# Kernel tuning notes

Measured on AMD Instinct MI355X. Metric: run time of the kernel, lower is better.

The kernel has to match this reference:

```python
import jax, jax.numpy as jnp
import numpy as np

B, N, C, H = 2, 2048, 128, 4
C4 = C // 4


def setup_inputs() -> dict:
    key = jax.random.key(0)
    ks = jax.random.split(key, 20)
    s = 0.02
    f = lambda k, sh: (jax.random.normal(k, sh, jnp.float32) * s)
    return {
        'x': jax.random.normal(ks[0], (B, N, C), jnp.float32),
        'A': jax.random.randint(ks[1], (N, N), 0, 2).astype(jnp.int32),
        'q_w1': f(ks[2], (C, C)), 'kv_w1': f(ks[3], (2 * C, C)),
        'proj_w1': f(ks[4], (C, C)), 'proj_b1': jnp.zeros((C,), jnp.float32),
        'q_w2': f(ks[5], (C, C)), 'kv_w2': f(ks[6], (2 * C, C)),
        'proj_w2': f(ks[7], (C, C)), 'proj_b2': jnp.zeros((C,), jnp.float32),
        'cq_w': f(ks[8], (C4, C)), 'cq_b': jnp.zeros((C4,), jnp.float32),
        'ck_w': f(ks[9], (C4, C)), 'ck_b': jnp.zeros((C4,), jnp.float32),
        'cv_w': f(ks[10], (C, C)), 'cv_b': jnp.zeros((C,), jnp.float32),
        'gc_w': f(ks[11], (C, C)), 'gc_b': jnp.zeros((C,), jnp.float32),
    }


def _attn_block(x, A, qw, kvw, pw, pb):
    # Attention._inner_attention + residual; qkv_bias=False, scale=head_dim**-0.5
    b, n, c = x.shape
    hd = c // H
    q = (x @ qw.T).reshape(b, n, H, hd).transpose(0, 2, 1, 3)          # [B,H,N,hd]
    kv = (x @ kvw.T).reshape(b, n, 2, H, hd).transpose(2, 0, 3, 1, 4)  # [2,B,H,N,hd]
    k, v = kv[0], kv[1]
    attn = jnp.einsum('bhnd,bhmd->bhnm', q, k) * (hd ** -0.5)
    attn = jnp.where(A[None, None] > 0, attn, jnp.float32(-9e15))
    attn = jax.nn.softmax(attn, axis=-1)
    out = jnp.einsum('bhnm,bhmd->bhnd', attn, v).transpose(0, 2, 1, 3).reshape(b, n, c)
    return out @ pw.T + pb + x


def _graph_conv(x, cq_w, cq_b, ck_w, ck_b, cv_w, cv_b, gc_w, gc_b):
    # GraphConvolution.forward: conv1d(k=1) QKV, softmax, topk scatter mask, masked softmax, bmm
    b, s, c = x.shape
    xp = x.transpose(0, 2, 1)                                          # [B,C,N]
    query = jnp.einsum('oi,bin->bon', cq_w, xp) + cq_b[:, None]        # [B,C/4,N]
    keyt = (jnp.einsum('oi,bin->bon', ck_w, xp) + ck_b[:, None]).transpose(0, 2, 1)  # [B,N,C/4]
    adj = jax.nn.softmax(jnp.einsum('bnc,bcm->bnm', keyt, query), axis=-1)           # [B,N,N]
    kk = int(s / 3 * 2)                                                # top-2/3 per row
    _, idx = jax.lax.top_k(adj, kk)                                    # [B,N,kk]
    mask = jnp.zeros(adj.shape, bool).at[
        jnp.arange(b)[:, None, None], jnp.arange(s)[None, :, None], idx].set(True)
    adj = jax.nn.softmax(jnp.where(mask, adj, -jnp.inf), axis=-1)
    value = (jnp.einsum('oi,bin->bon', cv_w, xp) + cv_b[:, None]).transpose(0, 2, 1)  # [B,N,C]
    support = value @ gc_w
    return jnp.einsum('bnm,bmc->bnc', adj, support) + gc_b


def reference(x, A, q_w1, kv_w1, proj_w1, proj_b1, q_w2, kv_w2, proj_w2, proj_b2,
              cq_w, cq_b, ck_w, ck_b, cv_w, cv_b, gc_w, gc_b):
    x = _attn_block(x, A, q_w1, kv_w1, proj_w1, proj_b1)
    x = _attn_block(x, A, q_w2, kv_w2, proj_w2, proj_b2)
    return _graph_conv(x, cq_w, cq_b, ck_w, ck_b, cv_w, cv_b, gc_w, gc_b)
```

## Files before the change

kernel.cpp:

```cpp
#include <hip/hip_runtime.h>
#include <hip/hip_bf16.h>
#include <math.h>

#define KK_TOP 1365

typedef __attribute__((ext_vector_type(8))) short v8s;
typedef __attribute__((ext_vector_type(4))) float f32x4;

#define MFMA16(a, b, c) __builtin_amdgcn_mfma_f32_16x16x32_bf16(a, b, c, 0, 0, 0)

__device__ inline float wave_max_f(float v) {
    #pragma unroll
    for (int m = 1; m < 64; m <<= 1) v = fmaxf(v, __shfl_xor(v, m));
    return v;
}
__device__ inline float wave_min_f(float v) {
    #pragma unroll
    for (int m = 1; m < 64; m <<= 1) v = fminf(v, __shfl_xor(v, m));
    return v;
}
__device__ inline float wave_sum_f(float v) {
    #pragma unroll
    for (int m = 1; m < 64; m <<= 1) v += __shfl_xor(v, m);
    return v;
}
__device__ inline unsigned short bf16bits(float x) {
    __hip_bfloat16 h = __float2bfloat16(x);
    return *reinterpret_cast<unsigned short*>(&h);
}

__global__ __launch_bounds__(256) void prep_k(
    const int* __restrict__ A, unsigned* __restrict__ Ab2,
    const float* __restrict__ cv_w, const float* __restrict__ cv_b,
    const float* __restrict__ gc_w, float* __restrict__ MT, float* __restrict__ B2,
    const float* __restrict__ x, short* __restrict__ xb,
    const float* __restrict__ q_w1, const float* __restrict__ kv_w1,
    const float* __restrict__ proj_w1, const float* __restrict__ q_w2,
    const float* __restrict__ kv_w2, const float* __restrict__ proj_w2,
    short* __restrict__ WALLb)
{
    const int bx = blockIdx.x;
    if (bx < 512) {
        const int lane = threadIdx.x & 63;
        const int w = threadIdx.x >> 6;
        const int row = bx * 4 + w;
        const int* rp = A + (size_t)row * 2048;
        for (int i = 0; i < 32; ++i) {
            unsigned long long bal = __ballot(rp[i * 64 + lane] > 0);
            if (lane == 0)  Ab2[(size_t)row * 64 + 2 * i]     = (unsigned)bal;
            if (lane == 32) Ab2[(size_t)row * 64 + 2 * i + 1] = (unsigned)(bal >> 32);
        }
    } else if (bx < 576) {
        const int b2 = bx - 512;
        const int c = b2 * 2 + (threadIdx.x >> 7);
        const int k = threadIdx.x & 127;
        float a = 0.f;
        #pragma unroll 4
        for (int i = 0; i < 128; ++i)
            a += cv_w[(size_t)i * 128 + k] * gc_w[(size_t)i * 128 + c];
        MT[(size_t)c * 128 + k] = a;
        if (b2 == 0 && threadIdx.x < 128) {
            float s = 0.f;
            #pragma unroll 4
            for (int i = 0; i < 128; ++i)
                s += cv_b[i] * gc_w[(size_t)i * 128 + threadIdx.x];
            B2[threadIdx.x] = s;
        }
    } else if (bx < 640) {
        const size_t base = (size_t)(bx - 576) * 8192;
        #pragma unroll 8
        for (int i = 0; i < 32; ++i) {
            size_t e = base + threadIdx.x + i * 256;
            xb[e] = (short)bf16bits(x[e]);
        }
    } else {
        const int base = (bx - 640) * 8192;
        const float* src; int off;
        if (base < 16384)       { src = q_w1;    off = base; }
        else if (base < 49152)  { src = kv_w1;   off = base - 16384; }
        else if (base < 65536)  { src = proj_w1; off = base - 49152; }
        else if (base < 81920)  { src = q_w2;    off = base - 65536; }
        else if (base < 114688) { src = kv_w2;   off = base - 81920; }
        else                    { src = proj_w2; off = base - 114688; }
        short* dst = WALLb + base;
        #pragma unroll 8
        for (int i = 0; i < 32; ++i) {
            int e = threadIdx.x + i * 256;
            dst[e] = (short)bf16bits(src[off + e]);
        }
    }
}

enum { MODE_QKV = 0, MODE_PROJ = 1 };

template <int MODE, bool EMITB>
__global__ __launch_bounds__(256) void mfma_gemm_k(
    const short* __restrict__ Xb, const short* __restrict__ Wb,
    const float* __restrict__ bias, const float* __restrict__ resid,
    short* __restrict__ Qo, short* __restrict__ Ko, short* __restrict__ Vto,
    float* __restrict__ Fo, short* __restrict__ Bo)
{
    const int tid = threadIdx.x;
    const int w = tid >> 6, lane = tid & 63;
    const int g = lane >> 4, c = lane & 15;
    const int m0 = blockIdx.x * 64 + w * 16;
    const int nbase = blockIdx.y * 64;

    v8s af[4];
    #pragma unroll
    for (int kk = 0; kk < 4; ++kk)
        af[kk] = *(const v8s*)(Xb + (size_t)(m0 + c) * 128 + kk * 32 + g * 8);

    for (int nf = 0; nf < 4; ++nf) {
        const int n0 = nbase + nf * 16;
        f32x4 acc = {0.f, 0.f, 0.f, 0.f};
        #pragma unroll
        for (int kk = 0; kk < 4; ++kk) {
            v8s bfr = *(const v8s*)(Wb + (size_t)(n0 + c) * 128 + kk * 32 + g * 8);
            acc = MFMA16(af[kk], bfr, acc);
        }
        const int ccol = n0 + c;
        #pragma unroll
        for (int r = 0; r < 4; ++r) {
            const int m = m0 + 4 * g + r;
            const int b = m >> 11, n = m & 2047;
            if (MODE == MODE_QKV) {
                unsigned short hv = bf16bits(acc[r]);
                if (ccol < 128) {
                    int hh = ccol >> 5, d = ccol & 31;
                    Qo[((size_t)(b * 4 + hh) * 2048 + n) * 32 + d] = (short)hv;
                } else if (ccol < 256) {
                    int c2 = ccol - 128; int hh = c2 >> 5, d = c2 & 31;
                    Ko[((size_t)(b * 4 + hh) * 2048 + n) * 32 + d] = (short)hv;
                } else {
                    int c2 = ccol - 256; int hh = c2 >> 5, d = c2 & 31;
                    Vto[((size_t)(b * 4 + hh) * 32 + d) * 2048 + n] = (short)hv;
                }
            } else {
                float v = acc[r] + bias[ccol] + resid[(size_t)m * 128 + ccol];
                Fo[(size_t)m * 128 + ccol] = v;
                if (EMITB) Bo[(size_t)m * 128 + ccol] = (short)bf16bits(v);
            }
        }
    }
}

__global__ __launch_bounds__(256) void graphmm_k(
    const float* __restrict__ X, const float* __restrict__ cq_w,
    const float* __restrict__ cq_b, const float* __restrict__ ck_w,
    const float* __restrict__ ck_b, const float* __restrict__ MT,
    const float* __restrict__ B2, float* __restrict__ QgT,
    float* __restrict__ Kg, __hip_bfloat16* __restrict__ SUPt)
{
    __shared__ __align__(16) float Xs[64][132];
    __shared__ __align__(16) float Ws[32][132];
    const int tid = threadIdx.x;
    const int m0 = blockIdx.x * 64;
    const int y = blockIdx.y;
    const float* W0   = (y == 0) ? cq_w : (y == 1) ? ck_w : MT;
    const float* bias = (y == 0) ? cq_b : (y == 1) ? ck_b : B2;
    const int n0 = (y < 2) ? 0 : (y - 2) * 32;

    #pragma unroll
    for (int i = 0; i < 32; ++i) {
        int idx = tid + i * 256;
        int row = idx >> 7, col = idx & 127;
        Xs[row][col] = X[(size_t)(m0 + row) * 128 + col];
    }
    #pragma unroll
    for (int i = 0; i < 16; ++i) {
        int idx = tid + i * 256;
        int r = idx >> 7, col = idx & 127;
        Ws[r][col] = W0[(size_t)(n0 + r) * 128 + col];
    }
    __syncthreads();

    const int r = tid >> 4;
    const int c = tid & 15;
    float acc[4][2] = {{0.f, 0.f}, {0.f, 0.f}, {0.f, 0.f}, {0.f, 0.f}};

    #pragma unroll
    for (int k = 0; k < 128; k += 4) {
        float4 w0 = *(const float4*)&Ws[c][k];
        float4 w1 = *(const float4*)&Ws[c + 16][k];
        #pragma unroll
        for (int i = 0; i < 4; ++i) {
            float4 xv = *(const float4*)&Xs[r + 16 * i][k];
            acc[i][0] += xv.x * w0.x + xv.y * w0.y + xv.z * w0.z + xv.w * w0.w;
            acc[i][1] += xv.x * w1.x + xv.y * w1.y + xv.z * w1.z + xv.w * w1.w;
        }
    }

    #pragma unroll
    for (int i = 0; i < 4; ++i) {
        int m = m0 + r + 16 * i;
        int b = m >> 11, n = m & 2047;
        #pragma unroll
        for (int jj = 0; jj < 2; ++jj) {
            int ccol = n0 + c + 16 * jj;
            float v = acc[i][jj];
            if (y == 0) {
                QgT[((size_t)b * 32 + ccol) * 2048 + n] = v + bias[ccol];
            } else if (y == 1) {
                Kg[(size_t)m * 32 + ccol] = v + bias[ccol];
            } else {
                SUPt[((size_t)b * 128 + ccol) * 2048 + n] = __float2bfloat16(v + bias[ccol]);
            }
        }
    }
}

__global__ __launch_bounds__(512, 8) void attn_mfma_k(
    const short* __restrict__ Qb, const short* __restrict__ Kb,
    const short* __restrict__ Vt, const unsigned* __restrict__ Ab2,
    short* __restrict__ Ob)
{
    __shared__ __align__(16) float OLDS[8][64][8];
    __shared__ float lred[8][16];

    const int tid = threadIdx.x;
    const int w = tid >> 6, lane = tid & 63;
    const int g = lane >> 4, c = lane & 15;
    const int bb = 4 * g;
    const int wg = blockIdx.x;
    const int b = wg >> 9, h = (wg >> 7) & 3, r0w = (wg & 127) << 4;
    const int bh = b * 4 + h;

    const v8s qf = *(const v8s*)(Qb + ((size_t)bh * 2048 + r0w + c) * 32 + g * 8);
    const short* Kp = Kb + (size_t)bh * 2048 * 32;
    const short* Vp = Vt + (size_t)bh * 32 * 2048;
    const unsigned* Mrow = Ab2 + (size_t)(r0w + c) * 64;

    f32x4 o0 = {0.f, 0.f, 0.f, 0.f}, o1 = {0.f, 0.f, 0.f, 0.f};
    float lsum = 0.f;
    const float SC2 = 0.25503487f;
    const bool lo = (g < 2);
    const int aA = (32 * (g & 1) + c) * 4;
    const int aB = aA + 64;

    #pragma unroll 2
    for (int t = 0; t < 8; ++t) {
        const int kt = t * 8 + w;
        const int key0 = kt * 32;
        v8s kf0 = *(const v8s*)(Kp + (size_t)(key0 + c) * 32 + g * 8);
        v8s kf1 = *(const v8s*)(Kp + (size_t)(key0 + 16 + c) * 32 + g * 8);
        unsigned mw = Mrow[kt];
        const f32x4 z = {0.f, 0.f, 0.f, 0.f};
        f32x4 s0 = MFMA16(kf0, qf, z);
        f32x4 s1 = MFMA16(kf1, qf, z);

        float p0[4], p1[4];
        #pragma unroll
        for (int r = 0; r < 4; ++r) {
            p0[r] = ((mw >> (bb + r)) & 1u)      ? exp2f(s0[r] * SC2) : 0.f;
            p1[r] = ((mw >> (16 + bb + r)) & 1u) ? exp2f(s1[r] * SC2) : 0.f;
        }
        lsum += p0[0] + p0[1] + p0[2] + p0[3] + p1[0] + p1[1] + p1[2] + p1[3];

        int w00 = (int)bf16bits(p0[0]) | ((int)bf16bits(p0[1]) << 16);
        int w01 = (int)bf16bits(p0[2]) | ((int)bf16bits(p0[3]) << 16);
        int w10 = (int)bf16bits(p1[0]) | ((int)bf16bits(p1[1]) << 16);
        int w11 = (int)bf16bits(p1[2]) | ((int)bf16bits(p1[3]) << 16);

        int e0, e1;
        union { int wv[4]; v8s v; } pf;
        e0 = __builtin_amdgcn_ds_bpermute(aA, w00);
        e1 = __builtin_amdgcn_ds_bpermute(aA, w10);
        pf.wv[0] = lo ? e0 : e1;
        e0 = __builtin_amdgcn_ds_bpermute(aA, w01);
        e1 = __builtin_amdgcn_ds_bpermute(aA, w11);
        pf.wv[1] = lo ? e0 : e1;
        e0 = __builtin_amdgcn_ds_bpermute(aB, w00);
        e1 = __builtin_amdgcn_ds_bpermute(aB, w10);
        pf.wv[2] = lo ? e0 : e1;
        e0 = __builtin_amdgcn_ds_bpermute(aB, w01);
        e1 = __builtin_amdgcn_ds_bpermute(aB, w11);
        pf.wv[3] = lo ? e0 : e1;

        v8s vf0 = *(const v8s*)(Vp + (size_t)c * 2048 + key0 + g * 8);
        v8s vf1 = *(const v8s*)(Vp + (size_t)(16 + c) * 2048 + key0 + g * 8);
        o0 = MFMA16(pf.v, vf0, o0);
        o1 = MFMA16(pf.v, vf1, o1);
    }

    lsum += __shfl_xor(lsum, 16);
    lsum += __shfl_xor(lsum, 32);

    *(f32x4*)&OLDS[w][lane][0] = o0;
    *(f32x4*)&OLDS[w][lane][4] = o1;
    if (lane < 16) lred[w][lane] = lsum;
    __syncthreads();

    if (tid < 64) {
        float iv[4];
        #pragma unroll
        for (int r = 0; r < 4; ++r) {
            float s = lred[0][bb + r];
            #pragma unroll
            for (int ww = 1; ww < 8; ++ww) s += lred[ww][bb + r];
            iv[r] = 1.f / s;
        }
        f32x4 a0 = *(f32x4*)&OLDS[0][lane][0];
        f32x4 a1 = *(f32x4*)&OLDS[0][lane][4];
        #pragma unroll
        for (int ww = 1; ww < 8; ++ww) {
            a0 += *(f32x4*)&OLDS[ww][lane][0];
            a1 += *(f32x4*)&OLDS[ww][lane][4];
        }
        #pragma unroll
        for (int r = 0; r < 4; ++r) {
            size_t base = ((size_t)b * 2048 + r0w + bb + r) * 128 + h * 32;
            Ob[base + c]      = (short)bf16bits(a0[r] * iv[r]);
            Ob[base + 16 + c] = (short)bf16bits(a1[r] * iv[r]);
        }
    }
}

__global__ __launch_bounds__(512, 4) void gadjout_k(
    const float* __restrict__ Kg, const float* __restrict__ QgT,
    const short* __restrict__ SUPt, const float* __restrict__ gcb,
    float* __restrict__ OUT)
{
    __shared__ __align__(16) float scores[8][2048];
    __shared__ float kg_s[8][32];

    const int tid = threadIdx.x;
    const int wg = blockIdx.x;
    const int b = wg >> 8;
    const int r0 = (wg & 255) << 3;

    if (tid < 256) {
        int rr = tid >> 5, d = tid & 31;
        kg_s[rr][d] = Kg[((size_t)b * 2048 + r0 + rr) * 32 + d];
    }
    __syncthreads();

    const float* Qp = QgT + (size_t)b * 32 * 2048;
    {
        float acc[8][4];
        #pragma unroll
        for (int rr = 0; rr < 8; ++rr)
            #pragma unroll
            for (int s = 0; s < 4; ++s) acc[rr][s] = 0.f;

        for (int dd = 0; dd < 32; ++dd) {
            float qv[8];
            #pragma unroll
            for (int rr = 0; rr < 8; ++rr) qv[rr] = kg_s[rr][dd];
            const float* kp = Qp + (size_t)dd * 2048 + tid;
            #pragma unroll
            for (int s = 0; s < 4; ++s) {
                float kv = kp[s * 512];
                #pragma unroll
                for (int rr = 0; rr < 8; ++rr)
                    acc[rr][s] = fmaf(qv[rr], kv, acc[rr][s]);
            }
        }
        #pragma unroll
        for (int s = 0; s < 4; ++s) {
            int jj = tid + 512 * s;
            #pragma unroll
            for (int rr = 0; rr < 8; ++rr) scores[rr][jj] = acc[rr][s];
        }
    }
    __syncthreads();

    const int lane = tid & 63, w = tid >> 6;
    const int g = lane >> 4, c = lane & 15;

    float mx = -3.0e38f;
    #pragma unroll
    for (int i = 0; i < 32; ++i) mx = fmaxf(mx, scores[w][lane + i * 64]);
    mx = wave_max_f(mx);

    float sm0 = 0.f;
    #pragma unroll
    for (int i = 0; i < 32; ++i) {
        float p = expf(scores[w][lane + i * 64] - mx);
        scores[w][lane + i * 64] = p;
        sm0 += p;
    }
    sm0 = wave_sum_f(sm0);
    const float ivw = 1.f / sm0;

    unsigned k_[32];
    float mxp = 0.f, mnp = 3.0e38f;
    #pragma unroll
    for (int i = 0; i < 32; ++i) {
        float p = scores[w][lane + i * 64] * ivw;
        k_[i] = __float_as_uint(p);
        mxp = fmaxf(mxp, p);
        mnp = fminf(mnp, p);
    }
    mxp = wave_max_f(mxp);
    mnp = wave_min_f(mnp);
    __syncthreads();

    unsigned thr = __float_as_uint(mnp);
    const unsigned umax = __float_as_uint(mxp);
    const unsigned diff = thr ^ umax;
    if (diff != 0u) {
        const int hb = 31 - __builtin_clz(diff);
        thr = (umax >> (hb + 1)) << (hb + 1);
        for (int bit = hb; bit >= 0; --bit) {
            unsigned cand = thr | (1u << bit);
            int cnt = 0;
            #pragma unroll
            for (int i = 0; i < 32; ++i)
                cnt += (int)__popcll(__ballot(k_[i] >= cand));
            if (cnt == KK_TOP) { thr = cand; break; }
            if (cnt > KK_TOP) thr = cand;
        }
    }

    int gt_c = 0;
    #pragma unroll
    for (int i = 0; i < 32; ++i)
        gt_c += (int)__popcll(__ballot(k_[i] > thr));
    const int need = KK_TOP - gt_c;

    unsigned keepmask = 0u;
    int running = 0;
    const unsigned long long ltmask = (lane == 0) ? 0ull : (~0ull >> (64 - lane));
    #pragma unroll
    for (int i = 0; i < 32; ++i) {
        bool tie = (k_[i] == thr);
        unsigned long long bal = __ballot(tie);
        int before = running + (int)__popcll(bal & ltmask);
        bool keep = (k_[i] > thr) || (tie && before < need);
        running += (int)__popcll(bal);
        if (keep) keepmask |= (1u << i);
    }

    const float LOG2E = 1.4426950408889634f;
    float sm = 0.f;
    #pragma unroll
    for (int i = 0; i < 32; ++i)
        if ((keepmask >> i) & 1u)
            sm += exp2f((__uint_as_float(k_[i]) - mxp) * LOG2E);
    sm = wave_sum_f(sm);
    const float ivs = 1.f / sm;

    unsigned short* adjl = (unsigned short*)&scores[0][0];
    const int wsw = (w & 7) << 3;
    #pragma unroll
    for (int i = 0; i < 32; ++i) {
        float o = ((keepmask >> i) & 1u)
                    ? exp2f((__uint_as_float(k_[i]) - mxp) * LOG2E) * ivs : 0.f;
        adjl[w * 2048 + ((lane + i * 64) ^ wsw)] = bf16bits(o);
    }
    __syncthreads();

    const short* adjs = (const short*)adjl;
    const short* Bp = SUPt + (size_t)b * 128 * 2048;
    const int csw = (c & 7) << 3;
    f32x4 oa = {0.f, 0.f, 0.f, 0.f};
    const v8s zero8 = {0, 0, 0, 0, 0, 0, 0, 0};
    #pragma unroll 2
    for (int kf = 0; kf < 64; ++kf) {
        const int k0 = kf * 32;
        v8s af2 = (c < 8) ? *(const v8s*)(adjs + (c * 2048 + ((k0 + g * 8) ^ csw)))
                          : zero8;
        v8s bf2 = *(const v8s*)(Bp + (size_t)(w * 16 + c) * 2048 + k0 + g * 8);
        oa = MFMA16(af2, bf2, oa);
    }
    if (g < 2) {
        const int col = w * 16 + c;
        const float bias = gcb[col];
        #pragma unroll
        for (int r = 0; r < 4; ++r)
            OUT[((size_t)b * 2048 + r0 + 4 * g + r) * 128 + col] = oa[r] + bias;
    }
}

extern "C" void kernel_launch(void* const* d_in, const int* in_sizes, int n_in,
                              void* d_out, int out_size, void* d_ws, size_t ws_size,
                              hipStream_t stream)
{
    const float* x       = (const float*)d_in[0];
    const int*   A       = (const int*)d_in[1];
    const float* q_w1    = (const float*)d_in[2];
    const float* kv_w1   = (const float*)d_in[3];
    const float* proj_w1 = (const float*)d_in[4];
    const float* proj_b1 = (const float*)d_in[5];
    const float* q_w2    = (const float*)d_in[6];
    const float* kv_w2   = (const float*)d_in[7];
    const float* proj_w2 = (const float*)d_in[8];
    const float* proj_b2 = (const float*)d_in[9];
    const float* cq_w    = (const float*)d_in[10];
    const float* cq_b    = (const float*)d_in[11];
    const float* ck_w    = (const float*)d_in[12];
    const float* ck_b    = (const float*)d_in[13];
    const float* cv_w    = (const float*)d_in[14];
    const float* cv_b    = (const float*)d_in[15];
    const float* gc_w    = (const float*)d_in[16];
    const float* gc_b    = (const float*)d_in[17];
    float* out = (float*)d_out;

    char* ws = (char*)d_ws;
    short*          Qb   = (short*)         (ws + 0);
    short*          Kb   = (short*)         (ws + 1048576);
    short*          Vt   = (short*)         (ws + 2097152);
    unsigned*       Ab2  = (unsigned*)      (ws + 19922944);
    short*          Ob   = (short*)         (ws + 20447232);
    float*          X1   = (float*)         (ws + 21495808);
    short*          X1b  = (short*)         (ws + 23592960);
    float*          X2   = (float*)         (ws + 24641536);
    float*          QgT  = (float*)         (ws + 26738688);
    float*          Kg   = (float*)         (ws + 27262976);
    __hip_bfloat16* SUPt = (__hip_bfloat16*)(ws + 27787264);
    float*          MT   = (float*)         (ws + 28835840);
    float*          B2   = (float*)         (ws + 28901376);
    short*          xb   = (short*)         (ws + 28901888);
    short*          WALLb= (short*)         (ws + 29950464);

    dim3 blk(256);
    dim3 blk512(512);

    hipLaunchKernelGGL(prep_k, dim3(656), blk, 0, stream,
                       A, Ab2, cv_w, cv_b, gc_w, MT, B2,
                       x, xb, q_w1, kv_w1, proj_w1, q_w2, kv_w2, proj_w2, WALLb);

    hipLaunchKernelGGL((mfma_gemm_k<MODE_QKV, false>), dim3(64, 6), blk, 0, stream,
                       xb, WALLb, nullptr, nullptr, Qb, Kb, Vt, nullptr, nullptr);
    hipLaunchKernelGGL(attn_mfma_k, dim3(1024), blk512, 0, stream,
                       Qb, Kb, Vt, Ab2, Ob);
    hipLaunchKernelGGL((mfma_gemm_k<MODE_PROJ, true>), dim3(64, 2), blk, 0, stream,
                       Ob, WALLb + 49152, proj_b1, x, nullptr, nullptr, nullptr, X1, X1b);

    hipLaunchKernelGGL((mfma_gemm_k<MODE_QKV, false>), dim3(64, 6), blk, 0, stream,
                       X1b, WALLb + 65536, nullptr, nullptr, Qb, Kb, Vt, nullptr, nullptr);
    hipLaunchKernelGGL(attn_mfma_k, dim3(1024), blk512, 0, stream,
                       Qb, Kb, Vt, Ab2, Ob);
    hipLaunchKernelGGL((mfma_gemm_k<MODE_PROJ, false>), dim3(64, 2), blk, 0, stream,
                       Ob, WALLb + 114688, proj_b2, X1, nullptr, nullptr, nullptr, X2, nullptr);

    hipLaunchKernelGGL(graphmm_k, dim3(64, 6), blk, 0, stream,
                       X2, cq_w, cq_b, ck_w, ck_b, MT, B2, QgT, Kg, SUPt);
    hipLaunchKernelGGL(gadjout_k, dim3(512), blk512, 0, stream,
                       Kg, QgT, (const short*)SUPt, gc_b, out);
}
```

Baseline: 275.9 us.

## Fuse all stages into one persistent kernel with a software grid barrier

The nine separate launches (prep, QKV/proj GEMMs, two attention passes, graph matmul, adjacency/output) become one persistent kernel of 256 blocks. The stages are separated by an atomic counter/generation grid barrier, and work is spread over wave-level tile loops. The first QKV GEMM now converts fp32 input to bf16 inline, so the separate x conversion pass is gone. The aim is to remove launch gaps and tail bubbles between the many small kernels. In exchange, each stage runs at a fixed grid of 256 blocks with lower occupancy (launch bounds 512,2), and every stage pays a spin-wait barrier.

```diff
diff --git a/kernel.cpp b/kernel.cpp
--- a/kernel.cpp
+++ b/kernel.cpp
@@ -3,6 +3,7 @@
 #include <math.h>
 
 #define KK_TOP 1365
+#define NB 256u
 
 typedef __attribute__((ext_vector_type(8))) short v8s;
 typedef __attribute__((ext_vector_type(4))) float f32x4;
@@ -29,202 +30,110 @@
     return *reinterpret_cast<unsigned short*>(&h);
 }
 
-__global__ __launch_bounds__(256) void prep_k(
-    const int* __restrict__ A, unsigned* __restrict__ Ab2,
-    const float* __restrict__ cv_w, const float* __restrict__ cv_b,
-    const float* __restrict__ gc_w, float* __restrict__ MT, float* __restrict__ B2,
-    const float* __restrict__ x, short* __restrict__ xb,
-    const float* __restrict__ q_w1, const float* __restrict__ kv_w1,
-    const float* __restrict__ proj_w1, const float* __restrict__ q_w2,
-    const float* __restrict__ kv_w2, const float* __restrict__ proj_w2,
-    short* __restrict__ WALLb)
+__device__ __forceinline__ void gsync(unsigned* cnt, unsigned* gen) {
+    __syncthreads();
+    if (threadIdx.x == 0) {
+        unsigned g = atomicAdd(gen, 0u);
+        __threadfence();
+        unsigned old = atomicAdd(cnt, 1u);
+        if (old == NB - 1u) {
+            atomicExch(cnt, 0u);
+            __threadfence();
+            atomicAdd(gen, 1u);
+        } else {
+            while (atomicAdd(gen, 0u) == g) __builtin_amdgcn_s_sleep(2);
+        }
+        __threadfence();
+    }
+    __syncthreads();
+}
+
+template <bool FROMF32>
+__device__ __forceinline__ void qkv_tiles(
+    const float* Xf, const short* Xbq, const short* Wb,
+    short* Qo, short* Ko, short* Vto, int wgid, int g, int c)
 {
-    const int bx = blockIdx.x;
-    if (bx < 512) {
-        const int lane = threadIdx.x & 63;
-        const int w = threadIdx.x >> 6;
-        const int row = bx * 4 + w;
-        const int* rp = A + (size_t)row * 2048;
-        for (int i = 0; i < 32; ++i) {
-            unsigned long long bal = __ballot(rp[i * 64 + lane] > 0);
-            if (lane == 0)  Ab2[(size_t)row * 64 + 2 * i]     = (unsigned)bal;
-            if (lane == 32) Ab2[(size_t)row * 64 + 2 * i + 1] = (unsigned)(bal >> 32);
-        }
-    } else if (bx < 576) {
-        const int b2 = bx - 512;
-        const int c = b2 * 2 + (threadIdx.x >> 7);
-        const int k = threadIdx.x & 127;
-        float a = 0.f;
-        #pragma unroll 4
-        for (int i = 0; i < 128; ++i)
-            a += cv_w[(size_t)i * 128 + k] * gc_w[(size_t)i * 128 + c];
-        MT[(size_t)c * 128 + k] = a;
-        if (b2 == 0 && threadIdx.x < 128) {
-            float s = 0.f;
-            #pragma unroll 4
-            for (int i = 0; i < 128; ++i)
-                s += cv_b[i] * gc_w[(size_t)i * 128 + threadIdx.x];
-            B2[threadIdx.x] = s;
-        }
-    } else if (bx < 640) {
-        const size_t base = (size_t)(bx - 576) * 8192;
-        #pragma unroll 8
-        for (int i = 0; i < 32; ++i) {
-            size_t e = base + threadIdx.x + i * 256;
-            xb[e] = (short)bf16bits(x[e]);
-        }
-    } else {
-        const int base = (bx - 640) * 8192;
-        const float* src; int off;
-        if (base < 16384)       { src = q_w1;    off = base; }
-        else if (base < 49152)  { src = kv_w1;   off = base - 16384; }
-        else if (base < 65536)  { src = proj_w1; off = base - 49152; }
-        else if (base < 81920)  { src = q_w2;    off = base - 65536; }
-        else if (base < 114688) { src = kv_w2;   off = base - 81920; }
-        else                    { src = proj_w2; off = base - 114688; }
-        short* dst = WALLb + base;
-        #pragma unroll 8
-        for (int i = 0; i < 32; ++i) {
-            int e = threadIdx.x + i * 256;
-            dst[e] = (short)bf16bits(src[off + e]);
-        }
-    }
-}
-
-enum { MODE_QKV = 0, MODE_PROJ = 1 };
-
-template <int MODE, bool EMITB>
-__global__ __launch_bounds__(256) void mfma_gemm_k(
-    const short* __restrict__ Xb, const short* __restrict__ Wb,
-    const float* __restrict__ bias, const float* __restrict__ resid,
-    short* __restrict__ Qo, short* __restrict__ Ko, short* __restrict__ Vto,
-    float* __restrict__ Fo, short* __restrict__ Bo)
+    for (int t = wgid; t < 6144; t += 2048) {
+        const int rt = t / 24, cf = t - rt * 24;
+        const int m0 = rt * 16, n0 = cf * 16;
+        v8s af[4];
+        if (FROMF32) {
+            #pragma unroll
+            for (int kk = 0; kk < 4; ++kk) {
+                const float* xp = Xf + (size_t)(m0 + c) * 128 + kk * 32 + g * 8;
+                union { short s[8]; v8s v; } u;
+                #pragma unroll
+                for (int j = 0; j < 8; ++j) u.s[j] = (short)bf16bits(xp[j]);
+                af[kk] = u.v;
+            }
+        } else {
+            #pragma unroll
+            for (int kk = 0; kk < 4; ++kk)
+                af[kk] = *(const v8s*)(Xbq + (size_t)(m0 + c) * 128 + kk * 32 + g * 8);
+        }
+        f32x4 acc = {0.f, 0.f, 0.f, 0.f};
+        #pragma unroll
+        for (int kk = 0; kk < 4; ++kk) {
+            v8s bfr = *(const v8s*)(Wb + (size_t)(n0 + c) * 128 + kk * 32 + g * 8);
+            acc = MFMA16(af[kk], bfr, acc);
+        }
+        const int ccol = n0 + c;
+        #pragma unroll
+        for (int r = 0; r < 4; ++r) {
+            const int m = m0 + 4 * g + r;
+            const int b = m >> 11, n = m & 2047;
+            unsigned short hv = bf16bits(acc[r]);
+            if (ccol < 128) {
+                int hh = ccol >> 5, d = ccol & 31;
+                Qo[((size_t)(b * 4 + hh) * 2048 + n) * 32 + d] = (short)hv;
+            } else if (ccol < 256) {
+                int c2 = ccol - 128; int hh = c2 >> 5, d = c2 & 31;
+                Ko[((size_t)(b * 4 + hh) * 2048 + n) * 32 + d] = (short)hv;
+            } else {
+                int c2 = ccol - 256; int hh = c2 >> 5, d = c2 & 31;
+                Vto[((size_t)(b * 4 + hh) * 32 + d) * 2048 + n] = (short)hv;
+            }
+        }
+    }
+}
+
+template <bool EMITB>
+__device__ __forceinline__ void proj_tiles(
+    const short* Xbq, const short* Wb, const float* bias, const float* resid,
+    float* Fo, short* Bo, int wgid, int g, int c)
 {
-    const int tid = threadIdx.x;
-    const int w = tid >> 6, lane = tid & 63;
-    const int g = lane >> 4, c = lane & 15;
-    const int m0 = blockIdx.x * 64 + w * 16;
-    const int nbase = blockIdx.y * 64;
-
+    const int t = wgid;
+    const int rt = t >> 3, cf = t & 7;
+    const int m0 = rt * 16, n0 = cf * 16;
     v8s af[4];
     #pragma unroll
     for (int kk = 0; kk < 4; ++kk)
-        af[kk] = *(const v8s*)(Xb + (size_t)(m0 + c) * 128 + kk * 32 + g * 8);
-
-    for (int nf = 0; nf < 4; ++nf) {
-        const int n0 = nbase + nf * 16;
-        f32x4 acc = {0.f, 0.f, 0.f, 0.f};
-        #pragma unroll
-        for (int kk = 0; kk < 4; ++kk) {
-            v8s bfr = *(const v8s*)(Wb + (size_t)(n0 + c) * 128 + kk * 32 + g * 8);
-            acc = MFMA16(af[kk], bfr, acc);
-        }
-        const int ccol = n0 + c;
-        #pragma unroll
-        for (int r = 0; r < 4; ++r) {
-            const int m = m0 + 4 * g + r;
-            const int b = m >> 11, n = m & 2047;
-            if (MODE == MODE_QKV) {
-                unsigned short hv = bf16bits(acc[r]);
-                if (ccol < 128) {
-                    int hh = ccol >> 5, d = ccol & 31;
-                    Qo[((size_t)(b * 4 + hh) * 2048 + n) * 32 + d] = (short)hv;
-                } else if (ccol < 256) {
-                    int c2 = ccol - 128; int hh = c2 >> 5, d = c2 & 31;
-                    Ko[((size_t)(b * 4 + hh) * 2048 + n) * 32 + d] = (short)hv;
-                } else {
-                    int c2 = ccol - 256; int hh = c2 >> 5, d = c2 & 31;
-                    Vto[((size_t)(b * 4 + hh) * 32 + d) * 2048 + n] = (short)hv;
-                }
-            } else {
-                float v = acc[r] + bias[ccol] + resid[(size_t)m * 128 + ccol];
-                Fo[(size_t)m * 128 + ccol] = v;
-                if (EMITB) Bo[(size_t)m * 128 + ccol] = (short)bf16bits(v);
-            }
-        }
-    }
-}
-
-__global__ __launch_bounds__(256) void graphmm_k(
-    const float* __restrict__ X, const float* __restrict__ cq_w,
-    const float* __restrict__ cq_b, const float* __restrict__ ck_w,
-    const float* __restrict__ ck_b, const float* __restrict__ MT,
-    const float* __restrict__ B2, float* __restrict__ QgT,
-    float* __restrict__ Kg, __hip_bfloat16* __restrict__ SUPt)
+        af[kk] = *(const v8s*)(Xbq + (size_t)(m0 + c) * 128 + kk * 32 + g * 8);
+    f32x4 acc = {0.f, 0.f, 0.f, 0.f};
+    #pragma unroll
+    for (int kk = 0; kk < 4; ++kk) {
+        v8s bfr = *(const v8s*)(Wb + (size_t)(n0 + c) * 128 + kk * 32 + g * 8);
+        acc = MFMA16(af[kk], bfr, acc);
+    }
+    const int ccol = n0 + c;
+    #pragma unroll
+    for (int r = 0; r < 4; ++r) {
+        const int m = m0 + 4 * g + r;
+        float v = acc[r] + bias[ccol] + resid[(size_t)m * 128 + ccol];
+        Fo[(size_t)m * 128 + ccol] = v;
+        if (EMITB) Bo[(size_t)m * 128 + ccol] = (short)bf16bits(v);
+    }
+}
+
+__device__ __forceinline__ void attn_vblock(
+    const short* Qb, const short* Kb, const short* Vt, const unsigned* Ab2,
+    short* Ob, float* OLDSf, float* lredf,
+    int vb, int tid, int w, int lane, int g, int c)
 {
-    __shared__ __align__(16) float Xs[64][132];
-    __shared__ __align__(16) float Ws[32][132];
-    const int tid = threadIdx.x;
-    const int m0 = blockIdx.x * 64;
-    const int y = blockIdx.y;
-    const float* W0   = (y == 0) ? cq_w : (y == 1) ? ck_w : MT;
-    const float* bias = (y == 0) ? cq_b : (y == 1) ? ck_b : B2;
-    const int n0 = (y < 2) ? 0 : (y - 2) * 32;
-
-    #pragma unroll
-    for (int i = 0; i < 32; ++i) {
-        int idx = tid + i * 256;
-        int row = idx >> 7, col = idx & 127;
-        Xs[row][col] = X[(size_t)(m0 + row) * 128 + col];
-    }
-    #pragma unroll
-    for (int i = 0; i < 16; ++i) {
-        int idx = tid + i * 256;
-        int r = idx >> 7, col = idx & 127;
-        Ws[r][col] = W0[(size_t)(n0 + r) * 128 + col];
-    }
+    const int b = vb >> 9, h = (vb >> 7) & 3, r0w = (vb & 127) << 4;
+    const int bh = b * 4 + h;
+    const int bb = 4 * g;
     __syncthreads();
-
-    const int r = tid >> 4;
-    const int c = tid & 15;
-    float acc[4][2] = {{0.f, 0.f}, {0.f, 0.f}, {0.f, 0.f}, {0.f, 0.f}};
-
-    #pragma unroll
-    for (int k = 0; k < 128; k += 4) {
-        float4 w0 = *(const float4*)&Ws[c][k];
-        float4 w1 = *(const float4*)&Ws[c + 16][k];
-        #pragma unroll
-        for (int i = 0; i < 4; ++i) {
-            float4 xv = *(const float4*)&Xs[r + 16 * i][k];
-            acc[i][0] += xv.x * w0.x + xv.y * w0.y + xv.z * w0.z + xv.w * w0.w;
-            acc[i][1] += xv.x * w1.x + xv.y * w1.y + xv.z * w1.z + xv.w * w1.w;
-        }
-    }
-
-    #pragma unroll
-    for (int i = 0; i < 4; ++i) {
-        int m = m0 + r + 16 * i;
-        int b = m >> 11, n = m & 2047;
-        #pragma unroll
-        for (int jj = 0; jj < 2; ++jj) {
-            int ccol = n0 + c + 16 * jj;
-            float v = acc[i][jj];
-            if (y == 0) {
-                QgT[((size_t)b * 32 + ccol) * 2048 + n] = v + bias[ccol];
-            } else if (y == 1) {
-                Kg[(size_t)m * 32 + ccol] = v + bias[ccol];
-            } else {
-                SUPt[((size_t)b * 128 + ccol) * 2048 + n] = __float2bfloat16(v + bias[ccol]);
-            }
-        }
-    }
-}
-
-__global__ __launch_bounds__(512, 8) void attn_mfma_k(
-    const short* __restrict__ Qb, const short* __restrict__ Kb,
-    const short* __restrict__ Vt, const unsigned* __restrict__ Ab2,
-    short* __restrict__ Ob)
-{
-    __shared__ __align__(16) float OLDS[8][64][8];
-    __shared__ float lred[8][16];
-
-    const int tid = threadIdx.x;
-    const int w = tid >> 6, lane = tid & 63;
-    const int g = lane >> 4, c = lane & 15;
-    const int bb = 4 * g;
-    const int wg = blockIdx.x;
-    const int b = wg >> 9, h = (wg >> 7) & 3, r0w = (wg & 127) << 4;
-    const int bh = b * 4 + h;
 
     const v8s qf = *(const v8s*)(Qb + ((size_t)bh * 2048 + r0w + c) * 32 + g * 8);
     const short* Kp = Kb + (size_t)bh * 2048 * 32;
@@ -239,8 +148,8 @@
     const int aB = aA + 64;
 
     #pragma unroll 2
-    for (int t = 0; t < 8; ++t) {
-        const int kt = t * 8 + w;
+    for (int tt = 0; tt < 8; ++tt) {
+        const int kt = tt * 8 + w;
         const int key0 = kt * 32;
         v8s kf0 = *(const v8s*)(Kp + (size_t)(key0 + c) * 32 + g * 8);
         v8s kf1 = *(const v8s*)(Kp + (size_t)(key0 + 16 + c) * 32 + g * 8);
@@ -286,26 +195,26 @@
     lsum += __shfl_xor(lsum, 16);
     lsum += __shfl_xor(lsum, 32);
 
-    *(f32x4*)&OLDS[w][lane][0] = o0;
-    *(f32x4*)&OLDS[w][lane][4] = o1;
-    if (lane < 16) lred[w][lane] = lsum;
+    *(f32x4*)&OLDSf[(w * 64 + lane) * 8 + 0] = o0;
+    *(f32x4*)&OLDSf[(w * 64 + lane) * 8 + 4] = o1;
+    if (lane < 16) lredf[w * 16 + lane] = lsum;
     __syncthreads();
 
     if (tid < 64) {
         float iv[4];
         #pragma unroll
         for (int r = 0; r < 4; ++r) {
-            float s = lred[0][bb + r];
-            #pragma unroll
-            for (int ww = 1; ww < 8; ++ww) s += lred[ww][bb + r];
+            float s = lredf[bb + r];
+            #pragma unroll
+            for (int ww = 1; ww < 8; ++ww) s += lredf[ww * 16 + bb + r];
             iv[r] = 1.f / s;
         }
-        f32x4 a0 = *(f32x4*)&OLDS[0][lane][0];
-        f32x4 a1 = *(f32x4*)&OLDS[0][lane][4];
+        f32x4 a0 = *(f32x4*)&OLDSf[lane * 8 + 0];
+        f32x4 a1 = *(f32x4*)&OLDSf[lane * 8 + 4];
         #pragma unroll
         for (int ww = 1; ww < 8; ++ww) {
-            a0 += *(f32x4*)&OLDS[ww][lane][0];
-            a1 += *(f32x4*)&OLDS[ww][lane][4];
+            a0 += *(f32x4*)&OLDSf[(ww * 64 + lane) * 8 + 0];
+            a1 += *(f32x4*)&OLDSf[(ww * 64 + lane) * 8 + 4];
         }
         #pragma unroll
         for (int r = 0; r < 4; ++r) {
@@ -316,160 +225,316 @@
     }
 }
 
-__global__ __launch_bounds__(512, 4) void gadjout_k(
-    const float* __restrict__ Kg, const float* __restrict__ QgT,
-    const short* __restrict__ SUPt, const float* __restrict__ gcb,
-    float* __restrict__ OUT)
+__global__ __launch_bounds__(512, 2) void mega_k(
+    const float* __restrict__ x, const int* __restrict__ A,
+    const float* __restrict__ q_w1, const float* __restrict__ kv_w1,
+    const float* __restrict__ proj_w1, const float* __restrict__ proj_b1,
+    const float* __restrict__ q_w2, const float* __restrict__ kv_w2,
+    const float* __restrict__ proj_w2, const float* __restrict__ proj_b2,
+    const float* __restrict__ cq_w, const float* __restrict__ cq_b,
+    const float* __restrict__ ck_w, const float* __restrict__ ck_b,
+    const float* __restrict__ cv_w, const float* __restrict__ cv_b,
+    const float* __restrict__ gc_w, const float* __restrict__ gc_b,
+    short* Qb, short* Kb, short* Vt, unsigned* Ab2, short* Ob,
+    float* X1, short* X1b, float* X2,
+    float* QgT, float* Kg, __hip_bfloat16* SUPt, float* MT, float* B2,
+    short* WALLb, unsigned* bar, float* OUT)
 {
-    __shared__ __align__(16) float scores[8][2048];
-    __shared__ float kg_s[8][32];
-
+    __shared__ __align__(16) char smem_[66560];
+    unsigned* cnt = bar;
+    unsigned* gen = bar + 16;
+
+    const int bx = blockIdx.x;
     const int tid = threadIdx.x;
-    const int wg = blockIdx.x;
-    const int b = wg >> 8;
-    const int r0 = (wg & 255) << 3;
-
-    if (tid < 256) {
-        int rr = tid >> 5, d = tid & 31;
-        kg_s[rr][d] = Kg[((size_t)b * 2048 + r0 + rr) * 32 + d];
-    }
-    __syncthreads();
-
-    const float* Qp = QgT + (size_t)b * 32 * 2048;
+    const int w = tid >> 6, lane = tid & 63;
+    const int g = lane >> 4, c = lane & 15;
+    const int wgid = bx * 8 + w;
+
     {
-        float acc[8][4];
-        #pragma unroll
-        for (int rr = 0; rr < 8; ++rr)
-            #pragma unroll
-            for (int s = 0; s < 4; ++s) acc[rr][s] = 0.f;
-
-        for (int dd = 0; dd < 32; ++dd) {
-            float qv[8];
-            #pragma unroll
-            for (int rr = 0; rr < 8; ++rr) qv[rr] = kg_s[rr][dd];
-            const float* kp = Qp + (size_t)dd * 2048 + tid;
+        const int row = bx * 8 + w;
+        const int* rp = A + (size_t)row * 2048;
+        for (int i = 0; i < 32; ++i) {
+            unsigned long long bal = __ballot(rp[i * 64 + lane] > 0);
+            if (lane == 0)  Ab2[(size_t)row * 64 + 2 * i]     = (unsigned)bal;
+            if (lane == 32) Ab2[(size_t)row * 64 + 2 * i + 1] = (unsigned)(bal >> 32);
+        }
+    }
+    if (bx < 32) {
+        const int cc = bx * 4 + (tid >> 7);
+        const int k = tid & 127;
+        float a = 0.f;
+        #pragma unroll 4
+        for (int i = 0; i < 128; ++i)
+            a += cv_w[(size_t)i * 128 + k] * gc_w[(size_t)i * 128 + cc];
+        MT[(size_t)cc * 128 + k] = a;
+    }
+    if (bx == 32 && tid < 128) {
+        float s = 0.f;
+        #pragma unroll 4
+        for (int i = 0; i < 128; ++i)
+            s += cv_b[i] * gc_w[(size_t)i * 128 + tid];
+        B2[tid] = s;
+    }
+    if (bx >= 64 && bx < 80) {
+        const int base = (bx - 64) * 8192;
+        const float* src; int off;
+        if (base < 16384)       { src = q_w1;    off = base; }
+        else if (base < 49152)  { src = kv_w1;   off = base - 16384; }
+        else if (base < 65536)  { src = proj_w1; off = base - 49152; }
+        else if (base < 81920)  { src = q_w2;    off = base - 65536; }
+        else if (base < 114688) { src = kv_w2;   off = base - 81920; }
+        else                    { src = proj_w2; off = base - 114688; }
+        short* dst = WALLb + base;
+        #pragma unroll 8
+        for (int i = 0; i < 16; ++i) {
+            int e = tid + i * 512;
+            dst[e] = (short)bf16bits(src[off + e]);
+        }
+    }
+    gsync(cnt, gen);
+
+    qkv_tiles<true>(x, nullptr, WALLb, Qb, Kb, Vt, wgid, g, c);
+    gsync(cnt, gen);
+
+    {
+        float* OLDSf = (float*)smem_;
+        float* lredf = (float*)(smem_ + 16384);
+        for (int vi = 0; vi < 4; ++vi)
+            attn_vblock(Qb, Kb, Vt, Ab2, Ob, OLDSf, lredf,
+                        bx * 4 + vi, tid, w, lane, g, c);
+    }
+    gsync(cnt, gen);
+
+    proj_tiles<true>(Ob, WALLb + 49152, proj_b1, x, X1, X1b, wgid, g, c);
+    gsync(cnt, gen);
+
+    qkv_tiles<false>(nullptr, X1b, WALLb + 65536, Qb, Kb, Vt, wgid, g, c);
+    gsync(cnt, gen);
+
+    {
+        float* OLDSf = (float*)smem_;
+        float* lredf = (float*)(smem_ + 16384);
+        for (int vi = 0; vi < 4; ++vi)
+            attn_vblock(Qb, Kb, Vt, Ab2, Ob, OLDSf, lredf,
+                        bx * 4 + vi, tid, w, lane, g, c);
+    }
+    gsync(cnt, gen);
+
+    proj_tiles<false>(Ob, WALLb + 114688, proj_b2, X1, X2, nullptr, wgid, g, c);
+    gsync(cnt, gen);
+
+    for (int vb = bx; vb < 384; vb += 256) {
+        float (*Xs)[132] = (float(*)[132])smem_;
+        float (*Ws)[132] = (float(*)[132])(smem_ + 33792);
+        const bool act = (tid < 256);
+        const int m0 = (vb & 63) * 64;
+        const int y = vb >> 6;
+        const float* W0   = (y == 0) ? cq_w : (y == 1) ? ck_w : MT;
+        const float* bias = (y == 0) ? cq_b : (y == 1) ? ck_b : B2;
+        const int n0 = (y < 2) ? 0 : (y - 2) * 32;
+
+        __syncthreads();
+        if (act) {
+            #pragma unroll
+            for (int i = 0; i < 32; ++i) {
+                int idx = tid + i * 256;
+                int row = idx >> 7, col = idx & 127;
+                Xs[row][col] = X2[(size_t)(m0 + row) * 128 + col];
+            }
+            #pragma unroll
+            for (int i = 0; i < 16; ++i) {
+                int idx = tid + i * 256;
+                int r = idx >> 7, col = idx & 127;
+                Ws[r][col] = W0[(size_t)(n0 + r) * 128 + col];
+            }
+        }
+        __syncthreads();
+
+        if (act) {
+            const int r = tid >> 4;
+            const int cc = tid & 15;
+            float acc[4][2] = {{0.f, 0.f}, {0.f, 0.f}, {0.f, 0.f}, {0.f, 0.f}};
+
+            #pragma unroll
+            for (int k = 0; k < 128; k += 4) {
+                float4 w0 = *(const float4*)&Ws[cc][k];
+                float4 w1 = *(const float4*)&Ws[cc + 16][k];
+                #pragma unroll
+                for (int i = 0; i < 4; ++i) {
+                    float4 xv = *(const float4*)&Xs[r + 16 * i][k];
+                    acc[i][0] += xv.x * w0.x + xv.y * w0.y + xv.z * w0.z + xv.w * w0.w;
+                    acc[i][1] += xv.x * w1.x + xv.y * w1.y + xv.z * w1.z + xv.w * w1.w;
+                }
+            }
+
+            #pragma unroll
+            for (int i = 0; i < 4; ++i) {
+                int m = m0 + r + 16 * i;
+                int b = m >> 11, n = m & 2047;
+                #pragma unroll
+                for (int jj = 0; jj < 2; ++jj) {
+                    int ccol = n0 + cc + 16 * jj;
+                    float v = acc[i][jj];
+                    if (y == 0) {
+                        QgT[((size_t)b * 32 + ccol) * 2048 + n] = v + bias[ccol];
+                    } else if (y == 1) {
+                        Kg[(size_t)m * 32 + ccol] = v + bias[ccol];
+                    } else {
+                        SUPt[((size_t)b * 128 + ccol) * 2048 + n] = __float2bfloat16(v + bias[ccol]);
+                    }
+                }
+            }
+        }
+    }
+    gsync(cnt, gen);
+
+    for (int vb = bx; vb < 512; vb += 256) {
+        float (*scores)[2048] = (float(*)[2048])smem_;
+        float (*kg_s)[32] = (float(*)[32])(smem_ + 65536);
+        const int b = vb >> 8;
+        const int r0 = (vb & 255) << 3;
+
+        __syncthreads();
+        if (tid < 256) {
+            int rr = tid >> 5, d = tid & 31;
+            kg_s[rr][d] = Kg[((size_t)b * 2048 + r0 + rr) * 32 + d];
+        }
+        __syncthreads();
+
+        const float* Qp = QgT + (size_t)b * 32 * 2048;
+        {
+            float acc[8][4];
+            #pragma unroll
+            for (int rr = 0; rr < 8; ++rr)
+                #pragma unroll
+                for (int s = 0; s < 4; ++s) acc[rr][s] = 0.f;
+
+            for (int dd = 0; dd < 32; ++dd) {
+                float qv[8];
+                #pragma unroll
+                for (int rr = 0; rr < 8; ++rr) qv[rr] = kg_s[rr][dd];
+                const float* kp = Qp + (size_t)dd * 2048 + tid;
+                #pragma unroll
+                for (int s = 0; s < 4; ++s) {
+                    float kv = kp[s * 512];
+                    #pragma unroll
+                    for (int rr = 0; rr < 8; ++rr)
+                        acc[rr][s] = fmaf(qv[rr], kv, acc[rr][s]);
+                }
+            }
             #pragma unroll
             for (int s = 0; s < 4; ++s) {
-                float kv = kp[s * 512];
-                #pragma unroll
-                for (int rr = 0; rr < 8; ++rr)
-                    acc[rr][s] = fmaf(qv[rr], kv, acc[rr][s]);
-            }
-        }
-        #pragma unroll
-        for (int s = 0; s < 4; ++s) {
-            int jj = tid + 512 * s;
-            #pragma unroll
-            for (int rr = 0; rr < 8; ++rr) scores[rr][jj] = acc[rr][s];
-        }
-    }
-    __syncthreads();
-
-    const int lane = tid & 63, w = tid >> 6;
-    const int g = lane >> 4, c = lane & 15;
-
-    float mx = -3.0e38f;
-    #pragma unroll
-    for (int i = 0; i < 32; ++i) mx = fmaxf(mx, scores[w][lane + i * 64]);
-    mx = wave_max_f(mx);
-
-    float sm0 = 0.f;
-    #pragma unroll
-    for (int i = 0; i < 32; ++i) {
-        float p = expf(scores[w][lane + i * 64] - mx);
-        scores[w][lane + i * 64] = p;
-        sm0 += p;
-    }
-    sm0 = wave_sum_f(sm0);
-    const float ivw = 1.f / sm0;
-
-    unsigned k_[32];
-    float mxp = 0.f, mnp = 3.0e38f;
-    #pragma unroll
-    for (int i = 0; i < 32; ++i) {
-        float p = scores[w][lane + i * 64] * ivw;
-        k_[i] = __float_as_uint(p);
-        mxp = fmaxf(mxp, p);
-        mnp = fminf(mnp, p);
-    }
-    mxp = wave_max_f(mxp);
-    mnp = wave_min_f(mnp);
-    __syncthreads();
-
-    unsigned thr = __float_as_uint(mnp);
-    const unsigned umax = __float_as_uint(mxp);
-    const unsigned diff = thr ^ umax;
-    if (diff != 0u) {
-        const int hb = 31 - __builtin_clz(diff);
-        thr = (umax >> (hb + 1)) << (hb + 1);
-        for (int bit = hb; bit >= 0; --bit) {
-            unsigned cand = thr | (1u << bit);
-            int cnt = 0;
-            #pragma unroll
-            for (int i = 0; i < 32; ++i)
-                cnt += (int)__popcll(__ballot(k_[i] >= cand));
-            if (cnt == KK_TOP) { thr = cand; break; }
-            if (cnt > KK_TOP) thr = cand;
-        }
-    }
-
-    int gt_c = 0;
-    #pragma unroll
-    for (int i = 0; i < 32; ++i)
-        gt_c += (int)__popcll(__ballot(k_[i] > thr));
-    const int need = KK_TOP - gt_c;
-
-    unsigned keepmask = 0u;
-    int running = 0;
-    const unsigned long long ltmask = (lane == 0) ? 0ull : (~0ull >> (64 - lane));
-    #pragma unroll
-    for (int i = 0; i < 32; ++i) {
-        bool tie = (k_[i] == thr);
-        unsigned long long bal = __ballot(tie);
-        int before = running + (int)__popcll(bal & ltmask);
-        bool keep = (k_[i] > thr) || (tie && before < need);
-        running += (int)__popcll(bal);
-        if (keep) keepmask |= (1u << i);
-    }
-
-    const float LOG2E = 1.4426950408889634f;
-    float sm = 0.f;
-    #pragma unroll
-    for (int i = 0; i < 32; ++i)
-        if ((keepmask >> i) & 1u)
-            sm += exp2f((__uint_as_float(k_[i]) - mxp) * LOG2E);
-    sm = wave_sum_f(sm);
-    const float ivs = 1.f / sm;
-
-    unsigned short* adjl = (unsigned short*)&scores[0][0];
-    const int wsw = (w & 7) << 3;
-    #pragma unroll
-    for (int i = 0; i < 32; ++i) {
-        float o = ((keepmask >> i) & 1u)
-                    ? exp2f((__uint_as_float(k_[i]) - mxp) * LOG2E) * ivs : 0.f;
-        adjl[w * 2048 + ((lane + i * 64) ^ wsw)] = bf16bits(o);
-    }
-    __syncthreads();
-
-    const short* adjs = (const short*)adjl;
-    const short* Bp = SUPt + (size_t)b * 128 * 2048;
-    const int csw = (c & 7) << 3;
-    f32x4 oa = {0.f, 0.f, 0.f, 0.f};
-    const v8s zero8 = {0, 0, 0, 0, 0, 0, 0, 0};
-    #pragma unroll 2
-    for (int kf = 0; kf < 64; ++kf) {
-        const int k0 = kf * 32;
-        v8s af2 = (c < 8) ? *(const v8s*)(adjs + (c * 2048 + ((k0 + g * 8) ^ csw)))
-                          : zero8;
-        v8s bf2 = *(const v8s*)(Bp + (size_t)(w * 16 + c) * 2048 + k0 + g * 8);
-        oa = MFMA16(af2, bf2, oa);
-    }
-    if (g < 2) {
-        const int col = w * 16 + c;
-        const float bias = gcb[col];
-        #pragma unroll
-        for (int r = 0; r < 4; ++r)
-            OUT[((size_t)b * 2048 + r0 + 4 * g + r) * 128 + col] = oa[r] + bias;
+                int jj = tid + 512 * s;
+                #pragma unroll
+                for (int rr = 0; rr < 8; ++rr) scores[rr][jj] = acc[rr][s];
+            }
+        }
+        __syncthreads();
+
+        float mx = -3.0e38f;
+        #pragma unroll
+        for (int i = 0; i < 32; ++i) mx = fmaxf(mx, scores[w][lane + i * 64]);
+        mx = wave_max_f(mx);
+
+        float sm0 = 0.f;
+        #pragma unroll
+        for (int i = 0; i < 32; ++i) {
+            float p = expf(scores[w][lane + i * 64] - mx);
+            scores[w][lane + i * 64] = p;
+            sm0 += p;
+        }
+        sm0 = wave_sum_f(sm0);
+        const float ivw = 1.f / sm0;
+
+        unsigned k_[32];
+        float mxp = 0.f, mnp = 3.0e38f;
+        #pragma unroll
+        for (int i = 0; i < 32; ++i) {
+            float p = scores[w][lane + i * 64] * ivw;
+            k_[i] = __float_as_uint(p);
+            mxp = fmaxf(mxp, p);
+            mnp = fminf(mnp, p);
+        }
+        mxp = wave_max_f(mxp);
+        mnp = wave_min_f(mnp);
+        __syncthreads();
+
+        unsigned thr = __float_as_uint(mnp);
+        const unsigned umax = __float_as_uint(mxp);
+        const unsigned diff = thr ^ umax;
+        if (diff != 0u) {
+            const int hb = 31 - __builtin_clz(diff);
+            thr = (umax >> (hb + 1)) << (hb + 1);
+            for (int bit = hb; bit >= 0; --bit) {
+                unsigned cand = thr | (1u << bit);
+                int cntk = 0;
+                #pragma unroll
+                for (int i = 0; i < 32; ++i)
+                    cntk += (int)__popcll(__ballot(k_[i] >= cand));
+                if (cntk == KK_TOP) { thr = cand; break; }
+                if (cntk > KK_TOP) thr = cand;
+            }
+        }
+
+        int gt_c = 0;
+        #pragma unroll
+        for (int i = 0; i < 32; ++i)
+            gt_c += (int)__popcll(__ballot(k_[i] > thr));
+        const int need = KK_TOP - gt_c;
+
+        unsigned keepmask = 0u;
+        int running = 0;
+        const unsigned long long ltmask = (lane == 0) ? 0ull : (~0ull >> (64 - lane));
+        #pragma unroll
+        for (int i = 0; i < 32; ++i) {
+            bool tie = (k_[i] == thr);
+            unsigned long long bal = __ballot(tie);
+            int before = running + (int)__popcll(bal & ltmask);
+            bool keep = (k_[i] > thr) || (tie && before < need);
+            running += (int)__popcll(bal);
+            if (keep) keepmask |= (1u << i);
+        }
+
+        const float LOG2E = 1.4426950408889634f;
+        float sm = 0.f;
+        #pragma unroll
+        for (int i = 0; i < 32; ++i)
+            if ((keepmask >> i) & 1u)
+                sm += exp2f((__uint_as_float(k_[i]) - mxp) * LOG2E);
+        sm = wave_sum_f(sm);
+        const float ivs = 1.f / sm;
+
+        unsigned short* adjl = (unsigned short*)&scores[0][0];
+        const int wsw = (w & 7) << 3;
+        #pragma unroll
+        for (int i = 0; i < 32; ++i) {
+            float o = ((keepmask >> i) & 1u)
+                        ? exp2f((__uint_as_float(k_[i]) - mxp) * LOG2E) * ivs : 0.f;
+            adjl[w * 2048 + ((lane + i * 64) ^ wsw)] = bf16bits(o);
+        }
+        __syncthreads();
+
+        const short* adjs = (const short*)adjl;
+        const short* Bp = (const short*)SUPt + (size_t)b * 128 * 2048;
+        const int csw = (c & 7) << 3;
+        f32x4 oa = {0.f, 0.f, 0.f, 0.f};
+        const v8s zero8 = {0, 0, 0, 0, 0, 0, 0, 0};
+        #pragma unroll 2
+        for (int kf = 0; kf < 64; ++kf) {
+            const int k0 = kf * 32;
+            v8s af2 = (c < 8) ? *(const v8s*)(adjs + (c * 2048 + ((k0 + g * 8) ^ csw)))
+                              : zero8;
+            v8s bf2 = *(const v8s*)(Bp + (size_t)(w * 16 + c) * 2048 + k0 + g * 8);
+            oa = MFMA16(af2, bf2, oa);
+        }
+        if (g < 2) {
+            const int col = w * 16 + c;
+            const float bias = gc_b[col];
+            #pragma unroll
+            for (int r = 0; r < 4; ++r)
+                OUT[((size_t)b * 2048 + r0 + 4 * g + r) * 128 + col] = oa[r] + bias;
+        }
+        __syncthreads();
     }
 }
 
@@ -497,46 +562,29 @@
     const float* gc_b    = (const float*)d_in[17];
     float* out = (float*)d_out;
 
-    char* ws = (char*)d_ws;
-    short*          Qb   = (short*)         (ws + 0);
-    short*          Kb   = (short*)         (ws + 1048576);
-    short*          Vt   = (short*)         (ws + 2097152);
-    unsigned*       Ab2  = (unsigned*)      (ws + 19922944);
-    short*          Ob   = (short*)         (ws + 20447232);
-    float*          X1   = (float*)         (ws + 21495808);
-    short*          X1b  = (short*)         (ws + 23592960);
-    float*          X2   = (float*)         (ws + 24641536);
-    float*          QgT  = (float*)         (ws + 26738688);
-    float*          Kg   = (float*)         (ws + 27262976);
-    __hip_bfloat16* SUPt = (__hip_bfloat16*)(ws + 27787264);
-    float*          MT   = (float*)         (ws + 28835840);
-    float*          B2   = (float*)         (ws + 28901376);
-    short*          xb   = (short*)         (ws + 28901888);
-    short*          WALLb= (short*)         (ws + 29950464);
-
-    dim3 blk(256);
-    dim3 blk512(512);
-
-    hipLaunchKernelGGL(prep_k, dim3(656), blk, 0, stream,
-                       A, Ab2, cv_w, cv_b, gc_w, MT, B2,
-                       x, xb, q_w1, kv_w1, proj_w1, q_w2, kv_w2, proj_w2, WALLb);
-
-    hipLaunchKernelGGL((mfma_gemm_k<MODE_QKV, false>), dim3(64, 6), blk, 0, stream,
-                       xb, WALLb, nullptr, nullptr, Qb, Kb, Vt, nullptr, nullptr);
-    hipLaunchKernelGGL(attn_mfma_k, dim3(1024), blk512, 0, stream,
-                       Qb, Kb, Vt, Ab2, Ob);
-    hipLaunchKernelGGL((mfma_gemm_k<MODE_PROJ, true>), dim3(64, 2), blk, 0, stream,
-                       Ob, WALLb + 49152, proj_b1, x, nullptr, nullptr, nullptr, X1, X1b);
-
-    hipLaunchKernelGGL((mfma_gemm_k<MODE_QKV, false>), dim3(64, 6), blk, 0, stream,
-                       X1b, WALLb + 65536, nullptr, nullptr, Qb, Kb, Vt, nullptr, nullptr);
-    hipLaunchKernelGGL(attn_mfma_k, dim3(1024), blk512, 0, stream,
-                       Qb, Kb, Vt, Ab2, Ob);
-    hipLaunchKernelGGL((mfma_gemm_k<MODE_PROJ, false>), dim3(64, 2), blk, 0, stream,
-                       Ob, WALLb + 114688, proj_b2, X1, nullptr, nullptr, nullptr, X2, nullptr);
-
-    hipLaunchKernelGGL(graphmm_k, dim3(64, 6), blk, 0, stream,
-                       X2, cq_w, cq_b, ck_w, ck_b, MT, B2, QgT, Kg, SUPt);
-    hipLaunchKernelGGL(gadjout_k, dim3(512), blk512, 0, stream,
-                       Kg, QgT, (const short*)SUPt, gc_b, out);
-}
+    char* wsb = (char*)d_ws;
+    short*          Qb   = (short*)         (wsb + 0);
+    short*          Kb   = (short*)         (wsb + 1048576);
+    short*          Vt   = (short*)         (wsb + 2097152);
+    unsigned*       Ab2  = (unsigned*)      (wsb + 3145728);
+    short*          Ob   = (short*)         (wsb + 3670016);
+    float*          X1   = (float*)         (wsb + 4718592);
+    short*          X1b  = (short*)         (wsb + 6815744);
+    float*          X2   = (float*)         (wsb + 7864320);
+    float*          QgT  = (float*)         (wsb + 9961472);
+    float*          Kg   = (float*)         (wsb + 10485760);
+    __hip_bfloat16* SUPt = (__hip_bfloat16*)(wsb + 11010048);
+    float*          MT   = (float*)         (wsb + 12058624);
+    float*          B2   = (float*)         (wsb + 12124160);
+    short*          WALLb= (short*)         (wsb + 12125184);
+    unsigned*       bar  = (unsigned*)      (wsb + 12387328);
+
+    hipMemsetAsync((void*)bar, 0, 128, stream);
+
+    hipLaunchKernelGGL(mega_k, dim3(256), dim3(512), 0, stream,
+                       x, A, q_w1, kv_w1, proj_w1, proj_b1,
+                       q_w2, kv_w2, proj_w2, proj_b2,
+                       cq_w, cq_b, ck_w, ck_b, cv_w, cv_b, gc_w, gc_b,
+                       Qb, Kb, Vt, Ab2, Ob, X1, X1b, X2,
+                       QgT, Kg, SUPt, MT, B2, WALLb, bar, out);
+}
```

Result: slower. 627.1 us (+127.3%).
